# Kernel optimization log

Measured on AMD Instinct MI355X. Metric: run time of the kernel, lower is better.

Reference implementation:

```python
import jax, jax.numpy as jnp
import numpy as np
import math

D = 4096  # in_features, power of 2 (required by Hadamard transform)

def _hadamard_matrix(n):
    # normalized Hadamard matrix built by Sylvester construction, matches torch code
    H = np.array([[1.0]], dtype=np.float32)
    inv_sqrt2 = np.float32(1.0 / math.sqrt(2.0))
    while H.shape[0] < n:
        H = np.block([[H, H], [H, -H]]) * inv_sqrt2
    return jnp.asarray(H, dtype=jnp.float32)

def _ste(x, q):
    # straight-through estimator: forward = q, backward = identity w.r.t. x
    return x + jax.lax.stop_gradient(q - x)

def _quant_1bit(w):
    scale = jnp.max(jnp.abs(w))
    safe = jnp.where(scale > 0, scale, 1.0)
    wn = w / safe
    q = jnp.sign(wn)
    q = jnp.where(jnp.abs(wn) < 0.5, 0.0, q) * scale
    q = jnp.where(scale > 0, q, w)
    return _ste(w, q)

def _quant_kbit(x, bits):
    qmin = float(-(2 ** (bits - 1)))
    qmax = float(2 ** (bits - 1) - 1)
    xmin, xmax = jnp.min(x), jnp.max(x)
    scale = (xmax - xmin) / (qmax - qmin)
    zero_point = qmin - jnp.round(xmin / scale)
    q = jnp.clip(jnp.round(x / scale + zero_point), qmin, qmax)
    dq = scale * (q - zero_point)
    return _ste(x, dq)

def setup_inputs() -> dict:
    key = jax.random.key(0)
    k1, k2 = jax.random.split(key)
    B, S = 4, 2048
    x = jax.random.normal(k1, (B, S, D), dtype=jnp.float32)
    # xavier-uniform-ish init for square weight: bound = sqrt(6/(in+out))
    bound = math.sqrt(6.0 / (D + D))
    weight = jax.random.uniform(k2, (D, D), dtype=jnp.float32, minval=-bound, maxval=bound)
    bias = jnp.zeros((D,), dtype=jnp.float32)
    return {"x": x, "weight": weight, "bias": bias}

def reference(x, weight, bias):
    H = _hadamard_matrix(D)  # symmetric, orthogonal; kept explicit to match source
    # weight quantization (1.58-bit ternary with STE)
    wq = _quant_1bit(weight)
    # activation: Hadamard transform -> 4-bit STE quant -> inverse transform
    t = jnp.einsum('bsd,ed->bse', x, H)          # x @ H.T
    tq = _quant_kbit(t, 4)
    xq = jnp.einsum('bsd,de->bse', tq, H)        # tq @ (H.T).T = tq @ H
    # linear
    out = jnp.einsum('bsd,od->bso', xq, wq) + bias
    return out
```

## Files before the change

kernel.cpp:

```cpp
#include <hip/hip_runtime.h>
#include <hip/hip_bf16.h>
#include <stdint.h>


#define D_DIM 4096

typedef __attribute__((ext_vector_type(8))) short bf16x8;
typedef __attribute__((ext_vector_type(4))) float f32x4;

__device__ __forceinline__ unsigned f2ord(float f) {
  unsigned u = __float_as_uint(f);
  return (u & 0x80000000u) ? ~u : (u | 0x80000000u);
}
__device__ __forceinline__ float ord2f(unsigned k) {
  return (k & 0x80000000u) ? __uint_as_float(k & 0x7fffffffu) : __uint_as_float(~k);
}
__device__ __forceinline__ unsigned f2bf(float f) {
  unsigned u = __float_as_uint(f);
  return ((u + 0x7fffu + ((u >> 16) & 1u)) >> 16) & 0xffffu;
}


__global__ void k_init(unsigned* keys) {
  keys[0] = 0u;
  keys[1] = 0xFFFFFFFFu;
  keys[2] = 0u;
}

__global__ __launch_bounds__(256) void k_wabs(const float* __restrict__ W, unsigned* keys) {
  float m = 0.0f;
  const int n4 = (D_DIM * D_DIM) / 4;
  for (int i = blockIdx.x * 256 + threadIdx.x; i < n4; i += gridDim.x * 256) {
    float4 v = ((const float4*)W)[i];
    m = fmaxf(m, fmaxf(fmaxf(fabsf(v.x), fabsf(v.y)), fmaxf(fabsf(v.z), fabsf(v.w))));
  }
  #pragma unroll
  for (int off = 32; off; off >>= 1) m = fmaxf(m, __shfl_down(m, off));
  __shared__ float sm[4];
  if ((threadIdx.x & 63) == 0) sm[threadIdx.x >> 6] = m;
  __syncthreads();
  if (threadIdx.x == 0) {
    m = fmaxf(fmaxf(sm[0], sm[1]), fmaxf(sm[2], sm[3]));
    atomicMax(keys + 0, f2ord(m));
  }
}

__global__ __launch_bounds__(256) void k_quant_w(const float* __restrict__ W,
                                                 const unsigned* __restrict__ keys,
                                                 unsigned short* __restrict__ wq) {
  const float scale = ord2f(keys[0]);
  const int i = blockIdx.x * 256 + threadIdx.x;
  float4 v = ((const float4*)W)[i];
  ushort4 o;
  {
    float wn = v.x / scale;
    o.x = (fabsf(wn) < 0.5f) ? 0 : ((wn < 0.0f) ? 0xBF80u : 0x3F80u);
    wn = v.y / scale;
    o.y = (fabsf(wn) < 0.5f) ? 0 : ((wn < 0.0f) ? 0xBF80u : 0x3F80u);
    wn = v.z / scale;
    o.z = (fabsf(wn) < 0.5f) ? 0 : ((wn < 0.0f) ? 0xBF80u : 0x3F80u);
    wn = v.w / scale;
    o.w = (fabsf(wn) < 0.5f) ? 0 : ((wn < 0.0f) ? 0xBF80u : 0x3F80u);
  }
  ((ushort4*)wq)[i] = o;
}

__device__ __forceinline__ void fwht_lds(float* row, int tid) {
  #pragma unroll
  for (int s = 0; s < 12; ++s) {
    const int stride = 1 << s;
    #pragma unroll
    for (int bb = 0; bb < 8; ++bb) {
      const int b = tid + bb * 256;
      const int i = ((b >> s) << (s + 1)) | (b & (stride - 1));
      const int j = i | stride;
      const float a = row[i], c = row[j];
      row[i] = a + c;
      row[j] = a - c;
    }
    __syncthreads();
  }
}

__global__ __launch_bounds__(256) void k_fwht_minmax(const float* __restrict__ x,
                                                     unsigned* keys) {
  __shared__ float row[D_DIM];
  const int tid = threadIdx.x;
  const float* src = x + (size_t)blockIdx.x * D_DIM;
  #pragma unroll
  for (int i = 0; i < 4; ++i)
    ((float4*)row)[tid + i * 256] = ((const float4*)src)[tid + i * 256];
  __syncthreads();
  fwht_lds(row, tid);
  float mn = 1e30f, mx = -1e30f;
  #pragma unroll
  for (int i = 0; i < 16; ++i) {
    const float v = row[tid + i * 256] * (1.0f / 64.0f);
    mn = fminf(mn, v);
    mx = fmaxf(mx, v);
  }
  #pragma unroll
  for (int off = 32; off; off >>= 1) {
    mn = fminf(mn, __shfl_down(mn, off));
    mx = fmaxf(mx, __shfl_down(mx, off));
  }
  __shared__ float smn[4], smx[4];
  if ((tid & 63) == 0) { smn[tid >> 6] = mn; smx[tid >> 6] = mx; }
  __syncthreads();
  if (tid == 0) {
    mn = fminf(fminf(smn[0], smn[1]), fminf(smn[2], smn[3]));
    mx = fmaxf(fmaxf(smx[0], smx[1]), fmaxf(smx[2], smx[3]));
    atomicMin(keys + 1, f2ord(mn));
    atomicMax(keys + 2, f2ord(mx));
  }
}

__global__ __launch_bounds__(256) void k_quant_fwht(const float* __restrict__ x,
                                                    const unsigned* __restrict__ keys,
                                                    unsigned short* __restrict__ xq) {
  __shared__ float row[D_DIM];
  const int tid = threadIdx.x;
  const float* src = x + (size_t)blockIdx.x * D_DIM;
  #pragma unroll
  for (int i = 0; i < 4; ++i)
    ((float4*)row)[tid + i * 256] = ((const float4*)src)[tid + i * 256];
  __syncthreads();
  fwht_lds(row, tid);

  const float tmin = ord2f(keys[1]);
  const float tmax = ord2f(keys[2]);
  const float scale = (tmax - tmin) / 15.0f;
  const float zp = -8.0f - rintf(tmin / scale);
  #pragma unroll
  for (int i = 0; i < 16; ++i) {
    const int idx = tid + i * 256;
    const float t = row[idx] * (1.0f / 64.0f);
    float q = rintf(t / scale + zp);
    q = fminf(fmaxf(q, -8.0f), 7.0f);
    row[idx] = scale * (q - zp);
  }
  __syncthreads();
  fwht_lds(row, tid);

  unsigned short* dst = xq + (size_t)blockIdx.x * D_DIM;
  #pragma unroll
  for (int c = 0; c < 2; ++c) {
    const int id = c * 256 + tid;
    float4 v0 = ((const float4*)row)[id * 2];
    float4 v1 = ((const float4*)row)[id * 2 + 1];
    uint4 pk;
    pk.x = f2bf(v0.x * (1.0f / 64.0f)) | (f2bf(v0.y * (1.0f / 64.0f)) << 16);
    pk.y = f2bf(v0.z * (1.0f / 64.0f)) | (f2bf(v0.w * (1.0f / 64.0f)) << 16);
    pk.z = f2bf(v1.x * (1.0f / 64.0f)) | (f2bf(v1.y * (1.0f / 64.0f)) << 16);
    pk.w = f2bf(v1.z * (1.0f / 64.0f)) | (f2bf(v1.w * (1.0f / 64.0f)) << 16);
    ((uint4*)dst)[id] = pk;
  }
}

typedef const __attribute__((address_space(1))) unsigned int gu32;
typedef __attribute__((address_space(3))) unsigned int lu32;
#define GLL(g, l) __builtin_amdgcn_global_load_lds((gu32*)(g), (lu32*)(l), 16, 0, 0)

__global__ __launch_bounds__(256) void k_gemm(const unsigned short* __restrict__ Xq,
                                              const unsigned short* __restrict__ Wq,
                                              const unsigned* __restrict__ keys,
                                              const float* __restrict__ bias,
                                              float* __restrict__ out) {
  __shared__ unsigned short lA[128 * 32];
  __shared__ unsigned short lB[128 * 32];
  const int tid = threadIdx.x;
  const int wave = tid >> 6, lane = tid & 63;
  const int wr = wave >> 1, wc = wave & 1;
  const size_t rowA0 = (size_t)blockIdx.x * 128;
  const size_t rowB0 = (size_t)blockIdx.y * 128;

  const int e = wave * 512 + lane * 8;
  const int er = e >> 5, ec = e & 31;
  const unsigned short* gA0 = Xq + (rowA0 + er) * D_DIM + ec;
  const unsigned short* gA1 = Xq + (rowA0 + 64 + er) * D_DIM + ec;
  const unsigned short* gB0 = Wq + (rowB0 + er) * D_DIM + ec;
  const unsigned short* gB1 = Wq + (rowB0 + 64 + er) * D_DIM + ec;
  unsigned short* lA0 = &lA[wave * 512];
  unsigned short* lA1 = &lA[2048 + wave * 512];
  unsigned short* lB0 = &lB[wave * 512];
  unsigned short* lB1 = &lB[2048 + wave * 512];

  f32x4 acc[4][4] = {};

  for (int kt = 0; kt < D_DIM / 32; ++kt) {
    const int ko = kt * 32;
    GLL(gA0 + ko, lA0);
    GLL(gA1 + ko, lA1);
    GLL(gB0 + ko, lB0);
    GLL(gB1 + ko, lB1);
    __syncthreads();
    bf16x8 af[4], bfr[4];
    #pragma unroll
    for (int i = 0; i < 4; ++i)
      af[i] = *(const bf16x8*)&lA[(wr * 64 + i * 16 + (lane & 15)) * 32 + (lane >> 4) * 8];
    #pragma unroll
    for (int i = 0; i < 4; ++i)
      bfr[i] = *(const bf16x8*)&lB[(wc * 64 + i * 16 + (lane & 15)) * 32 + (lane >> 4) * 8];
    #pragma unroll
    for (int mi = 0; mi < 4; ++mi)
      #pragma unroll
      for (int ni = 0; ni < 4; ++ni)
        acc[mi][ni] = __builtin_amdgcn_mfma_f32_16x16x32_bf16(af[mi], bfr[ni], acc[mi][ni], 0, 0, 0);
    __syncthreads();
  }

  const float wscale = ord2f(keys[0]);
  #pragma unroll
  for (int mi = 0; mi < 4; ++mi)
    #pragma unroll
    for (int ni = 0; ni < 4; ++ni)
      #pragma unroll
      for (int r = 0; r < 4; ++r) {
        const size_t row = rowA0 + wr * 64 + mi * 16 + (lane >> 4) * 4 + r;
        const size_t col = rowB0 + wc * 64 + ni * 16 + (lane & 15);
        out[row * D_DIM + col] = acc[mi][ni][r] * wscale + bias[col];
      }
}

extern "C" void kernel_launch(void* const* d_in, const int* in_sizes, int n_in,
                              void* d_out, int out_size, void* d_ws, size_t ws_size,
                              hipStream_t stream) {
  const float* x    = (const float*)d_in[0];
  const float* W    = (const float*)d_in[1];
  const float* bias = (const float*)d_in[2];
  float* out = (float*)d_out;

  const int rows = in_sizes[0] / D_DIM;

  unsigned* keys = (unsigned*)d_ws;
  unsigned short* xq = (unsigned short*)((char*)d_ws + 256);
  unsigned short* wq = (unsigned short*)((char*)d_ws + 256 + (size_t)rows * D_DIM * 2);

  k_init<<<1, 1, 0, stream>>>(keys);
  k_wabs<<<1024, 256, 0, stream>>>(W, keys);
  k_fwht_minmax<<<rows, 256, 0, stream>>>(x, keys);
  k_quant_w<<<(D_DIM * D_DIM / 4) / 256, 256, 0, stream>>>(W, keys, wq);
  k_quant_fwht<<<rows, 256, 0, stream>>>(x, keys, xq);
  k_gemm<<<dim3(rows / 128, D_DIM / 128), 256, 0, stream>>>(xq, wq, keys, bias, out);
}
```

Before: 986.6 us.

## Register-resident FWHT with one wave per row and double-buffered GEMM LDS

The Hadamard transform kernels now use a single 64-lane wave per row. Each lane holds 64 values in registers and does the butterflies there, with one swizzled LDS transpose in place of twelve LDS passes, each ending in a block barrier. Separately, the GEMM main loop double-buffers its LDS tiles so the next K-tile's global-to-LDS loads are issued before the current tile's MFMAs. The costs are heavy register pressure in the FWHT kernels, possibly spilling, and twice the GEMM LDS footprint.

```diff
diff --git a/kernel.cpp b/kernel.cpp
--- a/kernel.cpp
+++ b/kernel.cpp
@@ -65,95 +65,129 @@
   ((ushort4*)wq)[i] = o;
 }
 
-__device__ __forceinline__ void fwht_lds(float* row, int tid) {
-  #pragma unroll
-  for (int s = 0; s < 12; ++s) {
-    const int stride = 1 << s;
-    #pragma unroll
-    for (int bb = 0; bb < 8; ++bb) {
-      const int b = tid + bb * 256;
-      const int i = ((b >> s) << (s + 1)) | (b & (stride - 1));
-      const int j = i | stride;
-      const float a = row[i], c = row[j];
-      row[i] = a + c;
-      row[j] = a - c;
-    }
-    __syncthreads();
-  }
-}
-
-__global__ __launch_bounds__(256) void k_fwht_minmax(const float* __restrict__ x,
-                                                     unsigned* keys) {
-  __shared__ float row[D_DIM];
-  const int tid = threadIdx.x;
-  const float* src = x + (size_t)blockIdx.x * D_DIM;
-  #pragma unroll
-  for (int i = 0; i < 4; ++i)
-    ((float4*)row)[tid + i * 256] = ((const float4*)src)[tid + i * 256];
-  __syncthreads();
-  fwht_lds(row, tid);
+
+__device__ __forceinline__ void bfly_rv(f32x4 v[16]) {
+  #pragma unroll
+  for (int b = 1; b < 16; b <<= 1)
+    #pragma unroll
+    for (int rv = 0; rv < 16; ++rv)
+      if (!(rv & b)) {
+        f32x4 a = v[rv], c = v[rv | b];
+        v[rv] = a + c;
+        v[rv | b] = a - c;
+      }
+  #pragma unroll
+  for (int rv = 0; rv < 16; ++rv) {
+    f32x4 a = v[rv];
+    f32x4 t = {a.x + a.y, a.x - a.y, a.z + a.w, a.z - a.w};
+    v[rv] = (f32x4){t.x + t.z, t.y + t.w, t.x - t.z, t.y - t.w};
+  }
+}
+
+__device__ __forceinline__ void bfly_m(float w[64]) {
+  #pragma unroll
+  for (int b = 1; b < 64; b <<= 1)
+    #pragma unroll
+    for (int m = 0; m < 64; ++m)
+      if (!(m & b)) {
+        float a = w[m], c = w[m | b];
+        w[m] = a + c;
+        w[m | b] = a - c;
+      }
+}
+
+__device__ __forceinline__ void xpose_v2w(float* lds, const f32x4 v[16], float w[64], int l) {
+  #pragma unroll
+  for (int rv = 0; rv < 16; ++rv)
+    *(f32x4*)&lds[rv * 256 + ((l ^ (rv & 7)) << 2)] = v[rv];
+  __syncthreads();
+  const int rvL = l >> 2, jL = l & 3;
+  #pragma unroll
+  for (int m = 0; m < 64; ++m)
+    w[m] = lds[rvL * 256 + ((m ^ (rvL & 7)) << 2) + jL];
+}
+
+__device__ __forceinline__ void xpose_w2v(float* lds, const float w[64], f32x4 v[16], int l) {
+  const int rvL = l >> 2, jL = l & 3;
+  #pragma unroll
+  for (int m = 0; m < 64; ++m)
+    lds[rvL * 256 + ((m ^ (rvL & 7)) << 2) + jL] = w[m];
+  __syncthreads();
+  #pragma unroll
+  for (int rv = 0; rv < 16; ++rv)
+    v[rv] = *(const f32x4*)&lds[rv * 256 + ((l ^ (rv & 7)) << 2)];
+}
+
+__global__ __launch_bounds__(64) void k_fwht_minmax(const float* __restrict__ x,
+                                                    unsigned* keys) {
+  __shared__ float lds[D_DIM];
+  const int l = threadIdx.x;
+  const f32x4* src = (const f32x4*)(x + (size_t)blockIdx.x * D_DIM);
+  f32x4 v[16];
+  #pragma unroll
+  for (int rv = 0; rv < 16; ++rv) v[rv] = src[rv * 64 + l];
+  bfly_rv(v);
+  float w[64];
+  xpose_v2w(lds, v, w, l);
+  bfly_m(w);
   float mn = 1e30f, mx = -1e30f;
   #pragma unroll
-  for (int i = 0; i < 16; ++i) {
-    const float v = row[tid + i * 256] * (1.0f / 64.0f);
-    mn = fminf(mn, v);
-    mx = fmaxf(mx, v);
+  for (int m = 0; m < 64; ++m) {
+    const float t = w[m] * (1.0f / 64.0f);
+    mn = fminf(mn, t);
+    mx = fmaxf(mx, t);
   }
   #pragma unroll
   for (int off = 32; off; off >>= 1) {
     mn = fminf(mn, __shfl_down(mn, off));
     mx = fmaxf(mx, __shfl_down(mx, off));
   }
-  __shared__ float smn[4], smx[4];
-  if ((tid & 63) == 0) { smn[tid >> 6] = mn; smx[tid >> 6] = mx; }
-  __syncthreads();
-  if (tid == 0) {
-    mn = fminf(fminf(smn[0], smn[1]), fminf(smn[2], smn[3]));
-    mx = fmaxf(fmaxf(smx[0], smx[1]), fmaxf(smx[2], smx[3]));
+  if (l == 0) {
     atomicMin(keys + 1, f2ord(mn));
     atomicMax(keys + 2, f2ord(mx));
   }
 }
 
-__global__ __launch_bounds__(256) void k_quant_fwht(const float* __restrict__ x,
-                                                    const unsigned* __restrict__ keys,
-                                                    unsigned short* __restrict__ xq) {
-  __shared__ float row[D_DIM];
-  const int tid = threadIdx.x;
-  const float* src = x + (size_t)blockIdx.x * D_DIM;
-  #pragma unroll
-  for (int i = 0; i < 4; ++i)
-    ((float4*)row)[tid + i * 256] = ((const float4*)src)[tid + i * 256];
-  __syncthreads();
-  fwht_lds(row, tid);
+__global__ __launch_bounds__(64) void k_quant_fwht(const float* __restrict__ x,
+                                                   const unsigned* __restrict__ keys,
+                                                   unsigned short* __restrict__ xq) {
+  __shared__ float lds[D_DIM];
+  const int l = threadIdx.x;
+  const f32x4* src = (const f32x4*)(x + (size_t)blockIdx.x * D_DIM);
+  f32x4 v[16];
+  #pragma unroll
+  for (int rv = 0; rv < 16; ++rv) v[rv] = src[rv * 64 + l];
+  bfly_rv(v);
+  float w[64];
+  xpose_v2w(lds, v, w, l);
+  bfly_m(w);
 
   const float tmin = ord2f(keys[1]);
   const float tmax = ord2f(keys[2]);
   const float scale = (tmax - tmin) / 15.0f;
   const float zp = -8.0f - rintf(tmin / scale);
   #pragma unroll
-  for (int i = 0; i < 16; ++i) {
-    const int idx = tid + i * 256;
-    const float t = row[idx] * (1.0f / 64.0f);
+  for (int m = 0; m < 64; ++m) {
+    const float t = w[m] * (1.0f / 64.0f);
     float q = rintf(t / scale + zp);
     q = fminf(fmaxf(q, -8.0f), 7.0f);
-    row[idx] = scale * (q - zp);
-  }
-  __syncthreads();
-  fwht_lds(row, tid);
-
-  unsigned short* dst = xq + (size_t)blockIdx.x * D_DIM;
-  #pragma unroll
-  for (int c = 0; c < 2; ++c) {
-    const int id = c * 256 + tid;
-    float4 v0 = ((const float4*)row)[id * 2];
-    float4 v1 = ((const float4*)row)[id * 2 + 1];
-    uint4 pk;
-    pk.x = f2bf(v0.x * (1.0f / 64.0f)) | (f2bf(v0.y * (1.0f / 64.0f)) << 16);
-    pk.y = f2bf(v0.z * (1.0f / 64.0f)) | (f2bf(v0.w * (1.0f / 64.0f)) << 16);
-    pk.z = f2bf(v1.x * (1.0f / 64.0f)) | (f2bf(v1.y * (1.0f / 64.0f)) << 16);
-    pk.w = f2bf(v1.z * (1.0f / 64.0f)) | (f2bf(v1.w * (1.0f / 64.0f)) << 16);
-    ((uint4*)dst)[id] = pk;
+    w[m] = scale * (q - zp);
+  }
+
+  bfly_m(w);
+  __syncthreads();
+  xpose_w2v(lds, w, v, l);
+  bfly_rv(v);
+
+  ushort4* dst = (ushort4*)(xq + (size_t)blockIdx.x * D_DIM);
+  #pragma unroll
+  for (int rv = 0; rv < 16; ++rv) {
+    ushort4 o;
+    o.x = (unsigned short)f2bf(v[rv].x * (1.0f / 64.0f));
+    o.y = (unsigned short)f2bf(v[rv].y * (1.0f / 64.0f));
+    o.z = (unsigned short)f2bf(v[rv].z * (1.0f / 64.0f));
+    o.w = (unsigned short)f2bf(v[rv].w * (1.0f / 64.0f));
+    dst[rv * 64 + l] = o;
   }
 }
 
@@ -166,8 +200,8 @@
                                               const unsigned* __restrict__ keys,
                                               const float* __restrict__ bias,
                                               float* __restrict__ out) {
-  __shared__ unsigned short lA[128 * 32];
-  __shared__ unsigned short lB[128 * 32];
+  __shared__ unsigned short lA[2][128 * 32];
+  __shared__ unsigned short lB[2][128 * 32];
   const int tid = threadIdx.x;
   const int wave = tid >> 6, lane = tid & 63;
   const int wr = wave >> 1, wc = wave & 1;
@@ -180,33 +214,44 @@
   const unsigned short* gA1 = Xq + (rowA0 + 64 + er) * D_DIM + ec;
   const unsigned short* gB0 = Wq + (rowB0 + er) * D_DIM + ec;
   const unsigned short* gB1 = Wq + (rowB0 + 64 + er) * D_DIM + ec;
-  unsigned short* lA0 = &lA[wave * 512];
-  unsigned short* lA1 = &lA[2048 + wave * 512];
-  unsigned short* lB0 = &lB[wave * 512];
-  unsigned short* lB1 = &lB[2048 + wave * 512];
 
   f32x4 acc[4][4] = {};
 
+  {
+    unsigned short* a = &lA[0][wave * 512];
+    unsigned short* b = &lB[0][wave * 512];
+    GLL(gA0, a);
+    GLL(gA1, a + 2048);
+    GLL(gB0, b);
+    GLL(gB1, b + 2048);
+  }
+  __syncthreads();
+
+  int cur = 0;
   for (int kt = 0; kt < D_DIM / 32; ++kt) {
-    const int ko = kt * 32;
-    GLL(gA0 + ko, lA0);
-    GLL(gA1 + ko, lA1);
-    GLL(gB0 + ko, lB0);
-    GLL(gB1 + ko, lB1);
-    __syncthreads();
+    if (kt + 1 < D_DIM / 32) {
+      const int ko = (kt + 1) * 32;
+      unsigned short* a = &lA[cur ^ 1][wave * 512];
+      unsigned short* b = &lB[cur ^ 1][wave * 512];
+      GLL(gA0 + ko, a);
+      GLL(gA1 + ko, a + 2048);
+      GLL(gB0 + ko, b);
+      GLL(gB1 + ko, b + 2048);
+    }
     bf16x8 af[4], bfr[4];
     #pragma unroll
     for (int i = 0; i < 4; ++i)
-      af[i] = *(const bf16x8*)&lA[(wr * 64 + i * 16 + (lane & 15)) * 32 + (lane >> 4) * 8];
+      af[i] = *(const bf16x8*)&lA[cur][(wr * 64 + i * 16 + (lane & 15)) * 32 + (lane >> 4) * 8];
     #pragma unroll
     for (int i = 0; i < 4; ++i)
-      bfr[i] = *(const bf16x8*)&lB[(wc * 64 + i * 16 + (lane & 15)) * 32 + (lane >> 4) * 8];
+      bfr[i] = *(const bf16x8*)&lB[cur][(wc * 64 + i * 16 + (lane & 15)) * 32 + (lane >> 4) * 8];
     #pragma unroll
     for (int mi = 0; mi < 4; ++mi)
       #pragma unroll
       for (int ni = 0; ni < 4; ++ni)
         acc[mi][ni] = __builtin_amdgcn_mfma_f32_16x16x32_bf16(af[mi], bfr[ni], acc[mi][ni], 0, 0, 0);
     __syncthreads();
+    cur ^= 1;
   }
 
   const float wscale = ord2f(keys[0]);
@@ -238,8 +283,8 @@
 
   k_init<<<1, 1, 0, stream>>>(keys);
   k_wabs<<<1024, 256, 0, stream>>>(W, keys);
-  k_fwht_minmax<<<rows, 256, 0, stream>>>(x, keys);
+  k_fwht_minmax<<<rows, 64, 0, stream>>>(x, keys);
   k_quant_w<<<(D_DIM * D_DIM / 4) / 256, 256, 0, stream>>>(W, keys, wq);
-  k_quant_fwht<<<rows, 256, 0, stream>>>(x, keys, xq);
+  k_quant_fwht<<<rows, 64, 0, stream>>>(x, keys, xq);
   k_gemm<<<dim3(rows / 128, D_DIM / 128), 256, 0, stream>>>(xq, wq, keys, bias, out);
 }
```

Result: faster. 875.5 us (-11.3%).
